# Kernel tuning notes

Measured on AMD Instinct MI355X. Metric: run time of the kernel, lower is better.

Reference implementation:

```python
import jax, jax.numpy as jnp
import numpy as np

B, N, DIM = 4, 4096, 1024
HEADS, DIM_HEAD, BSZ, EPS = 8, 64, 16, 1e-8
INNER = HEADS * DIM_HEAD


def setup_inputs() -> dict:
    key = jax.random.key(0)
    k1, k2, k3 = jax.random.split(key, 3)
    x = jax.random.normal(k1, (B, N, DIM), dtype=jnp.float32)
    # torch nn.Linear weights are [out, in]; scale ~ fan_in^-0.5 for stable exp()
    w_qkv = jax.random.normal(k2, (3 * INNER, DIM), dtype=jnp.float32) * (DIM ** -0.5)
    w_out = jax.random.normal(k3, (DIM, INNER), dtype=jnp.float32) * (INNER ** -0.5)
    b_out = jnp.zeros((DIM,), dtype=jnp.float32)
    return {"x": x, "w_qkv": w_qkv, "w_out": w_out, "b_out": b_out}


def _to_bh(t, b, n):
    # 'b n (h d) -> (b h) n d'
    return t.reshape(b, n, HEADS, DIM_HEAD).transpose(0, 2, 1, 3).reshape(b * HEADS, n, DIM_HEAD)


def _to_blocks(t):
    # 'b (n z) d -> b n z d'
    return t.reshape(t.shape[0], -1, BSZ, DIM_HEAD)


def _calc_Y_and_A(qb, kb, vb):
    S = jnp.einsum('bnid,bnjd->bnij', qb, kb)   # block-local scores
    A = jnp.exp(S)
    y = jnp.einsum('bnij,bnjd->bnid', A, vb)
    return y.reshape(y.shape[0], -1, DIM_HEAD), A.sum(-1).reshape(A.shape[0], -1)


def _hattention(x, w_qkv, w_out, b_out):
    b, n, _ = x.shape
    qkv = x @ w_qkv.T
    q, k, v = jnp.split(qkv, 3, axis=-1)
    q, k, v = (_to_bh(t, b, n) for t in (q, k, v))
    q = q * (DIM_HEAD ** -0.5)

    num_levels = int(np.log2(n // BSZ)) - 1
    qkvs = [(q, k, v)]
    for _ in range(num_levels):
        q = q.reshape(q.shape[0], -1, 2, DIM_HEAD).mean(axis=2)
        k = k.reshape(k.shape[0], -1, 2, DIM_HEAD).mean(axis=2)
        v = v.reshape(v.shape[0], -1, 2, DIM_HEAD).sum(axis=2)
        qkvs.append((q, k, v))
    top_level = qkvs[0]
    coarse_levels = qkvs[1:][::-1]  # coarsest first

    Ys = []
    for (ql, kl, vl) in coarse_levels:
        qb, kb, vb = map(_to_blocks, (ql, kl, vl))
        bh, nb = kb.shape[0], kb.shape[1]
        # flip sibling key blocks: 'b (n r) z d' with r=2 reversed
        kb = kb.reshape(bh, nb // 2, 2, BSZ, DIM_HEAD)[:, :, ::-1].reshape(bh, nb, BSZ, DIM_HEAD)
        Ys.append(_calc_Y_and_A(qb, kb, vb))
    Ys.append(_calc_Y_and_A(*map(_to_blocks, top_level)))

    Y, A = Ys[0]
    for y_l, a_l in Ys[1:]:
        Y = jnp.repeat(Y, 2, axis=1) + y_l
        A = jnp.repeat(A, 2, axis=1) + a_l

    out = Y / (A + EPS)[..., None]
    # '(b h) n d -> b n (h d)'
    out = out.reshape(b, HEADS, n, DIM_HEAD).transpose(0, 2, 1, 3).reshape(b, n, INNER)
    return out @ w_out.T + b_out


def reference(x, w_qkv, w_out, b_out):
    return _hattention(x, w_qkv, w_out, b_out)
```

## Files before the change

### kernel.cpp

```cpp
#include <hip/hip_runtime.h>
#include <hip/hip_bf16.h>


typedef __bf16 bf16x8 __attribute__((ext_vector_type(8)));
typedef float floatx4 __attribute__((ext_vector_type(4)));
typedef unsigned short ushortx8 __attribute__((ext_vector_type(8)));
typedef unsigned int uintx4 __attribute__((ext_vector_type(4)));

#define ROWS_PER_BH 8160

__device__ __forceinline__ void g2lds16(const void* g, void* l) {
  __builtin_amdgcn_global_load_lds(
      (const __attribute__((address_space(1))) void*)g,
      (__attribute__((address_space(3))) void*)l, 16, 0, 0);
}

__device__ __forceinline__ unsigned short f2bu(float x) {
  __hip_bfloat16 h = __float2bfloat16(x);
  return *(unsigned short*)&h;
}
__device__ __forceinline__ float bu2f(unsigned short u) {
  __hip_bfloat16 h = *(__hip_bfloat16*)&u;
  return __bfloat162float(h);
}

__global__ __launch_bounds__(256) void f2b3_kernel(const float* __restrict__ x,
                                                   const float* __restrict__ wq,
                                                   const float* __restrict__ wo,
                                                   __hip_bfloat16* __restrict__ xb,
                                                   __hip_bfloat16* __restrict__ wqb,
                                                   __hip_bfloat16* __restrict__ wob) {
  int i0 = (blockIdx.x * 256 + threadIdx.x) * 8;
  const float* s;
  __hip_bfloat16* d;
  if (i0 < 16777216) {
    s = x + i0; d = xb + i0;
  } else if (i0 < 16777216 + 1572864) {
    s = wq + (i0 - 16777216); d = wqb + (i0 - 16777216);
  } else {
    s = wo + (i0 - 16777216 - 1572864); d = wob + (i0 - 16777216 - 1572864);
  }
  float4 v0 = *(const float4*)s;
  float4 v1 = *(const float4*)(s + 4);
  ushortx8 o;
  o[0] = f2bu(v0.x); o[1] = f2bu(v0.y); o[2] = f2bu(v0.z); o[3] = f2bu(v0.w);
  o[4] = f2bu(v1.x); o[5] = f2bu(v1.y); o[6] = f2bu(v1.z); o[7] = f2bu(v1.w);
  *(ushortx8*)d = o;
}

template <int K>
__device__ __forceinline__ void gemm_core(const unsigned short* __restrict__ A,
                                          const unsigned short* __restrict__ B,
                                          unsigned short* ldsA, unsigned short* ldsB,
                                          int tM, int tN, floatx4 acc[4][4]) {
  const int tid = threadIdx.x;
  const int lane = tid & 63, w = tid >> 6;
  const int wm = w >> 1, wn = w & 1;
  const int lr = lane >> 3;
  const int gch = (lane & 7) ^ lr;
  const unsigned short* Ag = A + (size_t)(tM + w * 32 + lr) * K + gch * 8;
  const unsigned short* Bg = B + (size_t)(tN + w * 32 + lr) * K + gch * 8;
  unsigned short* lA = &ldsA[w * 2048 + lane * 8];
  unsigned short* lB = &ldsB[w * 2048 + lane * 8];

  const int rA = wm * 64 + (lane & 15);
  const int rB = wn * 64 + (lane & 15);
  const int quad = lane >> 4;
  const int sw = lane & 7;

  for (int kt = 0; kt < K; kt += 64) {
    __syncthreads();
#pragma unroll
    for (int c = 0; c < 4; c++) {
      g2lds16(Ag + (size_t)(c * 8) * K + kt, lA + c * 512);
      g2lds16(Bg + (size_t)(c * 8) * K + kt, lB + c * 512);
    }
    __syncthreads();
#pragma unroll
    for (int kk = 0; kk < 2; kk++) {
      bf16x8 af[4], bv[4];
#pragma unroll
      for (int i = 0; i < 4; i++)
        af[i] = *(const bf16x8*)&ldsA[(rA + i * 16) * 64 + (((kk * 4 + quad) ^ sw) * 8)];
#pragma unroll
      for (int j = 0; j < 4; j++)
        bv[j] = *(const bf16x8*)&ldsB[(rB + j * 16) * 64 + (((kk * 4 + quad) ^ sw) * 8)];
#pragma unroll
      for (int i = 0; i < 4; i++)
#pragma unroll
        for (int j = 0; j < 4; j++)
          acc[i][j] = __builtin_amdgcn_mfma_f32_16x16x32_bf16(af[i], bv[j], acc[i][j], 0, 0, 0);
    }
  }
}

__global__ __launch_bounds__(256) void gemm_qkv_kernel(
    const unsigned short* __restrict__ A,
    const unsigned short* __restrict__ B,
    __hip_bfloat16* __restrict__ qp, __hip_bfloat16* __restrict__ kp,
    __hip_bfloat16* __restrict__ vp, int tMoff) {
  __shared__ unsigned short ldsA[128 * 64];
  __shared__ unsigned short ldsB[128 * 64];
  const int lane = threadIdx.x & 63, w = threadIdx.x >> 6;
  const int wm = w >> 1, wn = w & 1;
  const int tM = tMoff + blockIdx.x * 128, tN = blockIdx.y * 128;

  floatx4 acc[4][4];
#pragma unroll
  for (int i = 0; i < 4; i++)
#pragma unroll
    for (int j = 0; j < 4; j++) acc[i][j] = (floatx4){0.f, 0.f, 0.f, 0.f};

  gemm_core<1024>(A, B, ldsA, ldsB, tM, tN, acc);

  const int quad = lane >> 4, m15 = lane & 15;
#pragma unroll
  for (int i = 0; i < 4; i++) {
#pragma unroll
    for (int j = 0; j < 4; j++) {
      const int c = tN + wn * 64 + j * 16 + m15;
      const int tensor = c >> 9;
      const int rem = c & 511;
      const int h = rem >> 6, d = rem & 63;
      __hip_bfloat16* dstbuf = (tensor == 0) ? qp : ((tensor == 1) ? kp : vp);
      const float scale = (tensor == 0) ? 0.125f : 1.0f;
#pragma unroll
      for (int r = 0; r < 4; r++) {
        const int m = tM + wm * 64 + i * 16 + quad * 4 + r;
        const int b = m >> 12, n = m & 4095;
        size_t dst = ((size_t)(b * 8 + h) * ROWS_PER_BH + n) * 64 + d;
        dstbuf[dst] = __float2bfloat16(acc[i][j][r] * scale);
      }
      float s4 = acc[i][j][0] + acc[i][j][1] + acc[i][j][2] + acc[i][j][3];
      s4 += __shfl_xor(s4, 16, 64);
      s4 += __shfl_xor(s4, 32, 64);
      if (quad == 0) {
        const int mrow = tM + wm * 64 + i * 16;
        const int b = mrow >> 12, n4 = (mrow & 4095) >> 4;
        const float val = (tensor == 0) ? s4 * (0.125f / 16.f)
                         : ((tensor == 1) ? s4 * (1.f / 16.f) : s4);
        dstbuf[((size_t)(b * 8 + h) * ROWS_PER_BH + 7680 + n4) * 64 + d] =
            __float2bfloat16(val);
      }
    }
  }
}

__global__ __launch_bounds__(256) void gemm_out_kernel(
    const unsigned short* __restrict__ A,
    const unsigned short* __restrict__ B,
    const float* __restrict__ bias, float* __restrict__ out) {
  __shared__ unsigned short ldsA[128 * 64];
  __shared__ unsigned short ldsB[128 * 64];
  const int lane = threadIdx.x & 63, w = threadIdx.x >> 6;
  const int wm = w >> 1, wn = w & 1;
  const int tM = blockIdx.x * 128, tN = blockIdx.y * 128;

  floatx4 acc[4][4];
#pragma unroll
  for (int i = 0; i < 4; i++)
#pragma unroll
    for (int j = 0; j < 4; j++) acc[i][j] = (floatx4){0.f, 0.f, 0.f, 0.f};

  gemm_core<512>(A, B, ldsA, ldsB, tM, tN, acc);

  const int quad = lane >> 4;
#pragma unroll
  for (int i = 0; i < 4; i++) {
#pragma unroll
    for (int j = 0; j < 4; j++) {
      const int c = tN + wn * 64 + j * 16 + (lane & 15);
      const float bb = bias[c];
#pragma unroll
      for (int r = 0; r < 4; r++) {
        const int m = tM + wm * 64 + i * 16 + quad * 4 + r;
        out[(size_t)m * 1024 + c] = acc[i][j][r] + bb;
      }
    }
  }
}

__device__ __forceinline__ int swzf(int r) { return (r ^ (r >> 3)) & 7; }
__device__ __forceinline__ int sidx(int r, int d) {
  return r * 64 + (((d >> 3) ^ swzf(r)) << 3) + (d & 7);
}
#define VT_SZ 1600

__global__ __launch_bounds__(512, 1) void coarse47_kernel(
    const unsigned short* __restrict__ qp, const unsigned short* __restrict__ kp,
    const unsigned short* __restrict__ vp, __hip_bfloat16* __restrict__ yall,
    float* __restrict__ aall) {
  __shared__ __align__(16) unsigned short qs[256 * 64];
  __shared__ __align__(16) unsigned short ks[256 * 64];
  __shared__ __align__(16) unsigned short vs[256 * 64];
  __shared__ __align__(16) unsigned short vT[8][VT_SZ];

  const int tid = threadIdx.x;
  const int w = tid >> 6, lane = tid & 63;
  const int m = lane & 15, q = lane >> 4;
  const int bh = blockIdx.x;
  const size_t base = (size_t)bh * ROWS_PER_BH;
  const size_t g0 = (base + 7680) * 64;

  unsigned short* vtw = vT[w];

  {
    const int srow = tid >> 3;
    const int sch = (tid & 7) ^ swzf(srow);
    const size_t gofs = (size_t)srow * 64 + sch * 8;
#pragma unroll
    for (int it = 0; it < 4; it++) {
      const size_t gi = g0 + (size_t)it * 4096 + gofs;
      g2lds16(qp + gi, &qs[it * 4096 + tid * 8]);
      g2lds16(kp + gi, &ks[it * 4096 + tid * 8]);
      g2lds16(vp + gi, &vs[it * 4096 + tid * 8]);
    }
  }
  __syncthreads();

  auto attn_block = [&](int level, int blk, bool flip, floatx4 yout[4]) -> float {
    const int kb = flip ? (blk ^ 1) : blk;
    const int Rq = (blk * 16 + m) << level;
    const int Rk = (kb * 16 + m) << level;
    const bf16x8 ka0 = *(const bf16x8*)&ks[sidx(Rk, q * 8)];
    const bf16x8 ka1 = *(const bf16x8*)&ks[sidx(Rk, 32 + q * 8)];
    const bf16x8 qb0 = *(const bf16x8*)&qs[sidx(Rq, q * 8)];
    const bf16x8 qb1 = *(const bf16x8*)&qs[sidx(Rq, 32 + q * 8)];
    const ushortx8 v0 = *(const ushortx8*)&vs[sidx(Rq, q * 16)];
    const ushortx8 v1 = *(const ushortx8*)&vs[sidx(Rq, q * 16 + 8)];
#pragma unroll
    for (int j = 0; j < 8; j++) vtw[q * 16 + (q * 16 + j) * 24 + m] = v0[j];
#pragma unroll
    for (int j = 0; j < 8; j++) vtw[q * 16 + (q * 16 + 8 + j) * 24 + m] = v1[j];

    floatx4 s = (floatx4){0.f, 0.f, 0.f, 0.f};
    s = __builtin_amdgcn_mfma_f32_16x16x32_bf16(ka0, qb0, s, 0, 0, 0);
    s = __builtin_amdgcn_mfma_f32_16x16x32_bf16(ka1, qb1, s, 0, 0, 0);

    unsigned short pb0 = f2bu(__expf(s[0])), pb1 = f2bu(__expf(s[1]));
    unsigned short pb2 = f2bu(__expf(s[2])), pb3 = f2bu(__expf(s[3]));
    float asum = bu2f(pb0) + bu2f(pb1) + bu2f(pb2) + bu2f(pb3);
    asum += __shfl_xor(asum, 16, 64);
    asum += __shfl_xor(asum, 32, 64);

    unsigned int d0 = (unsigned int)pb0 | ((unsigned int)pb1 << 16);
    unsigned int d1 = (unsigned int)pb2 | ((unsigned int)pb3 << 16);
    const int s0l = m + 32 * (q & 1);
    unsigned int u0 = __shfl(d0, s0l, 64);
    unsigned int u1 = __shfl(d1, s0l, 64);
    unsigned int u2 = __shfl(d0, s0l + 16, 64);
    unsigned int u3 = __shfl(d1, s0l + 16, 64);
    union { uintx4 i; bf16x8 b; } pau;
    pau.i = (q < 2) ? (uintx4){u0, u1, u2, u3} : (uintx4){0u, 0u, 0u, 0u};
    const bf16x8 pa = pau.b;

#pragma unroll
    for (int cc = 0; cc < 4; cc++) {
      union { uintx4 i; bf16x8 b; } bvu;
      bvu.i = (uintx4){0u, 0u, 0u, 0u};
      if (q < 2) bvu.b = *(const bf16x8*)&vtw[cc * 16 + (cc * 16 + m) * 24 + q * 8];
      floatx4 y = (floatx4){0.f, 0.f, 0.f, 0.f};
      y = __builtin_amdgcn_mfma_f32_16x16x32_bf16(pa, bvu.b, y, 0, 0, 0);
      yout[cc] = y;
    }
    return asum;
  };

  auto pyr = [&](int l) {
    const int nOut = 256 >> l;
    for (int e = tid; e < nOut * 32; e += 512) {
      const int i = e >> 5, dp = (e & 31) * 2;
      const int ra = i << l, rb = ra + (1 << (l - 1));
      const int ia = sidx(ra, dp), ib = sidx(rb, dp);
      unsigned short q0 = f2bu(0.5f * (bu2f(qs[ia]) + bu2f(qs[ib])));
      unsigned short q1 = f2bu(0.5f * (bu2f(qs[ia + 1]) + bu2f(qs[ib + 1])));
      unsigned short k0 = f2bu(0.5f * (bu2f(ks[ia]) + bu2f(ks[ib])));
      unsigned short k1 = f2bu(0.5f * (bu2f(ks[ia + 1]) + bu2f(ks[ib + 1])));
      unsigned short v0 = f2bu(bu2f(vs[ia]) + bu2f(vs[ib]));
      unsigned short v1 = f2bu(bu2f(vs[ia + 1]) + bu2f(vs[ib + 1]));
      qs[ia] = q0; qs[ia + 1] = q1;
      ks[ia] = k0; ks[ia + 1] = k1;
      vs[ia] = v0; vs[ia + 1] = v1;
    }
  };

  auto emit = [&](int ro, int blk, const floatx4 yt[4], float a) {
    const size_t arow = base + ro + blk * 16;
    if (q == 0) aall[arow + m] = a;
#pragma unroll
    for (int cc = 0; cc < 4; cc++)
#pragma unroll
      for (int r = 0; r < 4; r++)
        yall[(arow + q * 4 + r) * 64 + cc * 16 + m] = __float2bfloat16(yt[cc][r]);
  };

  {
    floatx4 yt[4];
#pragma unroll
    for (int t = 0; t < 2; t++) {
      const int blk = w + t * 8;
      float a = attn_block(0, blk, true, yt);
      emit(7680, blk, yt, a);
    }
  }
  __syncthreads();
  pyr(1);
  __syncthreads();
  {
    floatx4 yt[4];
    float a = attn_block(1, w, true, yt);
    emit(7936, w, yt, a);
  }
  __syncthreads();
  pyr(2);
  __syncthreads();
  if (w < 4) {
    floatx4 yt[4];
    float a = attn_block(2, w, true, yt);
    emit(8064, w, yt, a);
  }
  __syncthreads();
  pyr(3);
  __syncthreads();
  if (w < 2) {
    floatx4 yt[4];
    float a = attn_block(3, w, true, yt);
    emit(8128, w, yt, a);
  }
}

__global__ __launch_bounds__(512, 1) void fused03_kernel(
    const unsigned short* __restrict__ qp, const unsigned short* __restrict__ kp,
    const unsigned short* __restrict__ vp, const unsigned short* __restrict__ yall,
    const float* __restrict__ aall, __hip_bfloat16* __restrict__ Ub) {
  __shared__ __align__(16) unsigned short qs[256 * 64];
  __shared__ __align__(16) unsigned short ks[256 * 64];
  __shared__ __align__(16) unsigned short vs[256 * 64];
  __shared__ unsigned short ylds[224 * 72];
  __shared__ float alds[480];
  __shared__ __align__(16) unsigned short vT[8][VT_SZ];

  const int tid = threadIdx.x;
  const int w = tid >> 6, lane = tid & 63;
  const int m = lane & 15, q = lane >> 4;
  const int c = blockIdx.x, bh = blockIdx.y;
  const size_t base = (size_t)bh * ROWS_PER_BH;
  const size_t g0 = (base + c * 256) * 64;

  unsigned short* vtw = vT[w];

  {
    const int srow = tid >> 3;
    const int sch = (tid & 7) ^ swzf(srow);
    const size_t gofs = (size_t)srow * 64 + sch * 8;
#pragma unroll
    for (int it = 0; it < 4; it++) {
      const size_t gi = g0 + (size_t)it * 4096 + gofs;
      g2lds16(qp + gi, &qs[it * 4096 + tid * 8]);
      g2lds16(kp + gi, &ks[it * 4096 + tid * 8]);
      g2lds16(vp + gi, &vs[it * 4096 + tid * 8]);
    }
  }
  __syncthreads();

  auto attn_block = [&](int level, int blk, bool flip, floatx4 yout[4]) -> float {
    const int kb = flip ? (blk ^ 1) : blk;
    const int Rq = (blk * 16 + m) << level;
    const int Rk = (kb * 16 + m) << level;
    const bf16x8 ka0 = *(const bf16x8*)&ks[sidx(Rk, q * 8)];
    const bf16x8 ka1 = *(const bf16x8*)&ks[sidx(Rk, 32 + q * 8)];
    const bf16x8 qb0 = *(const bf16x8*)&qs[sidx(Rq, q * 8)];
    const bf16x8 qb1 = *(const bf16x8*)&qs[sidx(Rq, 32 + q * 8)];
    const ushortx8 v0 = *(const ushortx8*)&vs[sidx(Rq, q * 16)];
    const ushortx8 v1 = *(const ushortx8*)&vs[sidx(Rq, q * 16 + 8)];
#pragma unroll
    for (int j = 0; j < 8; j++) vtw[q * 16 + (q * 16 + j) * 24 + m] = v0[j];
#pragma unroll
    for (int j = 0; j < 8; j++) vtw[q * 16 + (q * 16 + 8 + j) * 24 + m] = v1[j];

    floatx4 s = (floatx4){0.f, 0.f, 0.f, 0.f};
    s = __builtin_amdgcn_mfma_f32_16x16x32_bf16(ka0, qb0, s, 0, 0, 0);
    s = __builtin_amdgcn_mfma_f32_16x16x32_bf16(ka1, qb1, s, 0, 0, 0);

    unsigned short pb0 = f2bu(__expf(s[0])), pb1 = f2bu(__expf(s[1]));
    unsigned short pb2 = f2bu(__expf(s[2])), pb3 = f2bu(__expf(s[3]));
    float asum = bu2f(pb0) + bu2f(pb1) + bu2f(pb2) + bu2f(pb3);
    asum += __shfl_xor(asum, 16, 64);
    asum += __shfl_xor(asum, 32, 64);

    unsigned int d0 = (unsigned int)pb0 | ((unsigned int)pb1 << 16);
    unsigned int d1 = (unsigned int)pb2 | ((unsigned int)pb3 << 16);
    const int s0l = m + 32 * (q & 1);
    unsigned int u0 = __shfl(d0, s0l, 64);
    unsigned int u1 = __shfl(d1, s0l, 64);
    unsigned int u2 = __shfl(d0, s0l + 16, 64);
    unsigned int u3 = __shfl(d1, s0l + 16, 64);
    union { uintx4 i; bf16x8 b; } pau;
    pau.i = (q < 2) ? (uintx4){u0, u1, u2, u3} : (uintx4){0u, 0u, 0u, 0u};
    const bf16x8 pa = pau.b;

#pragma unroll
    for (int cc = 0; cc < 4; cc++) {
      union { uintx4 i; bf16x8 b; } bvu;
      bvu.i = (uintx4){0u, 0u, 0u, 0u};
      if (q < 2) bvu.b = *(const bf16x8*)&vtw[cc * 16 + (cc * 16 + m) * 24 + q * 8];
      floatx4 y = (floatx4){0.f, 0.f, 0.f, 0.f};
      y = __builtin_amdgcn_mfma_f32_16x16x32_bf16(pa, bvu.b, y, 0, 0, 0);
      yout[cc] = y;
    }
    return asum;
  };

  auto pyr = [&](int l) {
    const int nOut = 256 >> l;
    for (int e = tid; e < nOut * 32; e += 512) {
      const int i = e >> 5, dp = (e & 31) * 2;
      const int ra = i << l, rb = ra + (1 << (l - 1));
      const int ia = sidx(ra, dp), ib = sidx(rb, dp);
      unsigned short q0 = f2bu(0.5f * (bu2f(qs[ia]) + bu2f(qs[ib])));
      unsigned short q1 = f2bu(0.5f * (bu2f(qs[ia + 1]) + bu2f(qs[ib + 1])));
      unsigned short k0 = f2bu(0.5f * (bu2f(ks[ia]) + bu2f(ks[ib])));
      unsigned short k1 = f2bu(0.5f * (bu2f(ks[ia + 1]) + bu2f(ks[ib + 1])));
      unsigned short v0 = f2bu(bu2f(vs[ia]) + bu2f(vs[ib]));
      unsigned short v1 = f2bu(bu2f(vs[ia + 1]) + bu2f(vs[ib + 1]));
      qs[ia] = q0; qs[ia + 1] = q1;
      ks[ia] = k0; ks[ia + 1] = k1;
      vs[ia] = v0; vs[ia + 1] = v1;
    }
  };

  floatx4 y0reg[2][4];
#pragma unroll
  for (int t = 0; t < 2; t++) {
    const int blk = w + t * 8;
    float a0 = attn_block(0, blk, false, y0reg[t]);
    if (q == 0) alds[224 + blk * 16 + m] = a0;
  }
  __syncthreads();

  pyr(1);
  __syncthreads();
  {
    floatx4 yt[4];
    const int blk = w;
    float a = attn_block(1, blk, true, yt);
    if (q == 0) alds[blk * 16 + m] = a;
#pragma unroll
    for (int cc = 0; cc < 4; cc++)
#pragma unroll
      for (int r = 0; r < 4; r++)
        ylds[(blk * 16 + q * 4 + r) * 72 + cc * 16 + m] = f2bu(yt[cc][r]);
  }
  __syncthreads();
  pyr(2);
  __syncthreads();
  if (w < 4) {
    floatx4 yt[4];
    const int blk = w;
    float a = attn_block(2, blk, true, yt);
    if (q == 0) alds[128 + blk * 16 + m] = a;
#pragma unroll
    for (int cc = 0; cc < 4; cc++)
#pragma unroll
      for (int r = 0; r < 4; r++)
        ylds[(128 + blk * 16 + q * 4 + r) * 72 + cc * 16 + m] = f2bu(yt[cc][r]);
  }
  __syncthreads();
  pyr(3);
  __syncthreads();
  if (w < 2) {
    floatx4 yt[4];
    const int blk = w;
    float a = attn_block(3, blk, true, yt);
    if (q == 0) alds[192 + blk * 16 + m] = a;
#pragma unroll
    for (int cc = 0; cc < 4; cc++)
#pragma unroll
      for (int r = 0; r < 4; r++)
        ylds[(192 + blk * 16 + q * 4 + r) * 72 + cc * 16 + m] = f2bu(yt[cc][r]);
  }
  __syncthreads();

  const int bO = bh >> 3, hO = bh & 7;
#pragma unroll
  for (int t = 0; t < 2; t++) {
    const int blk = w + t * 8;
    const int i4 = c * 16 + blk;
    const size_t r4 = base + 7680 + i4;
    const size_t r5 = base + 7936 + (i4 >> 1);
    const size_t r6 = base + 8064 + (i4 >> 2);
    const size_t r7 = base + 8128 + (i4 >> 3);
    const float acoarse = aall[r4] + aall[r5] + aall[r6] + aall[r7];

    float inv[4];
#pragma unroll
    for (int r = 0; r < 4; r++) {
      const int row = blk * 16 + q * 4 + r;
      const float atot = alds[224 + row] + alds[row >> 1] +
                         alds[128 + (row >> 2)] + alds[192 + (row >> 3)] +
                         acoarse + 1e-8f;
      inv[r] = 1.0f / atot;
    }

#pragma unroll
    for (int cc = 0; cc < 4; cc++) {
      const int col = cc * 16 + m;
      const float yc = bu2f(yall[r4 * 64 + col]) + bu2f(yall[r5 * 64 + col]) +
                       bu2f(yall[r6 * 64 + col]) + bu2f(yall[r7 * 64 + col]);
#pragma unroll
      for (int r = 0; r < 4; r++) {
        const int row = blk * 16 + q * 4 + r;
        const float num = y0reg[t][cc][r] + bu2f(ylds[(row >> 1) * 72 + col]) +
                          bu2f(ylds[(128 + (row >> 2)) * 72 + col]) +
                          bu2f(ylds[(192 + (row >> 3)) * 72 + col]) + yc;
        Ub[((size_t)bO * 4096 + c * 256 + row) * 512 + hO * 64 + col] =
            __float2bfloat16(num * inv[r]);
      }
    }
  }
}

extern "C" void kernel_launch(void* const* d_in, const int* in_sizes, int n_in,
                              void* d_out, int out_size, void* d_ws, size_t ws_size,
                              hipStream_t stream) {
  const float* x     = (const float*)d_in[0];
  const float* w_qkv = (const float*)d_in[1];
  const float* w_out = (const float*)d_in[2];
  const float* b_out = (const float*)d_in[3];
  float* out = (float*)d_out;

  char* ws = (char*)d_ws;
  __hip_bfloat16* xb    = (__hip_bfloat16*)(ws + 0);
  __hip_bfloat16* wqkvb = (__hip_bfloat16*)(ws + 33554432);
  __hip_bfloat16* wob   = (__hip_bfloat16*)(ws + 36700160);
  __hip_bfloat16* qp    = (__hip_bfloat16*)(ws + 37748736);
  __hip_bfloat16* kp    = (__hip_bfloat16*)(ws + 71172096);
  __hip_bfloat16* vp    = (__hip_bfloat16*)(ws + 104595456);
  __hip_bfloat16* yall  = (__hip_bfloat16*)(ws + 138018816);
  float* aall           = (float*)(ws + 171442176);
  __hip_bfloat16* Ub    = (__hip_bfloat16*)(ws + 172486656);

  f2b3_kernel<<<9216, 256, 0, stream>>>(x, w_qkv, w_out, xb, wqkvb, wob);

  gemm_qkv_kernel<<<dim3(64, 12), 256, 0, stream>>>(
      (const unsigned short*)xb, (const unsigned short*)wqkvb, qp, kp, vp, 0);
  gemm_qkv_kernel<<<dim3(64, 12), 256, 0, stream>>>(
      (const unsigned short*)xb, (const unsigned short*)wqkvb, qp, kp, vp, 8192);

  coarse47_kernel<<<32, 512, 0, stream>>>(
      (const unsigned short*)qp, (const unsigned short*)kp,
      (const unsigned short*)vp, yall, aall);

  fused03_kernel<<<dim3(16, 32), 512, 0, stream>>>(
      (const unsigned short*)qp, (const unsigned short*)kp,
      (const unsigned short*)vp, (const unsigned short*)yall, aall, Ub);

  gemm_out_kernel<<<dim3(128, 8), 256, 0, stream>>>(
      (const unsigned short*)Ub, (const unsigned short*)wob, b_out, out);
}
```

Baseline: 271.1 us.

## Compute pyramid levels 1-3 in QKV GEMM epilogue and read them from global

The QKV GEMM epilogue now writes pooled q/k/v for levels 1, 2 and 3 (pairs, quads, octets) as well as level 4, using partial sums of the accumulator fragments. The fused03 kernel therefore drops its LDS staging of 256 rows and the in-LDS pyramid reductions with their barriers, and loads each level's blocks straight from global memory. This frees most of its shared memory, so launch bounds allow 4 blocks per CU, and levels 2 and 3 now run concurrently on different waves. The two QKV GEMM launches are merged into one. In exchange the GEMM epilogue issues more scattered bf16 stores, and the pooled values are formed from fp32 accumulators rather than from bf16-rounded rows.

```diff
diff --git a/kernel.cpp b/kernel.cpp
--- a/kernel.cpp
+++ b/kernel.cpp
@@ -94,16 +94,18 @@
   }
 }
 
+__constant__ int LVLOFF[8] = {0, 4096, 6144, 7168, 7680, 7936, 8064, 8128};
+
 __global__ __launch_bounds__(256) void gemm_qkv_kernel(
     const unsigned short* __restrict__ A,
     const unsigned short* __restrict__ B,
     __hip_bfloat16* __restrict__ qp, __hip_bfloat16* __restrict__ kp,
-    __hip_bfloat16* __restrict__ vp, int tMoff) {
+    __hip_bfloat16* __restrict__ vp) {
   __shared__ unsigned short ldsA[128 * 64];
   __shared__ unsigned short ldsB[128 * 64];
   const int lane = threadIdx.x & 63, w = threadIdx.x >> 6;
   const int wm = w >> 1, wn = w & 1;
-  const int tM = tMoff + blockIdx.x * 128, tN = blockIdx.y * 128;
+  const int tM = blockIdx.x * 128, tN = blockIdx.y * 128;
 
   floatx4 acc[4][4];
 #pragma unroll
@@ -131,16 +133,35 @@
         size_t dst = ((size_t)(b * 8 + h) * ROWS_PER_BH + n) * 64 + d;
         dstbuf[dst] = __float2bfloat16(acc[i][j][r] * scale);
       }
-      float s4 = acc[i][j][0] + acc[i][j][1] + acc[i][j][2] + acc[i][j][3];
-      s4 += __shfl_xor(s4, 16, 64);
-      s4 += __shfl_xor(s4, 32, 64);
+      const float s2a = acc[i][j][0] + acc[i][j][1];
+      const float s2b = acc[i][j][2] + acc[i][j][3];
+      const float s4v = s2a + s2b;
+      const float s8v = s4v + __shfl_xor(s4v, 16, 64);
+      const float s16v = s8v + __shfl_xor(s8v, 32, 64);
+      const int mg = tM + wm * 64 + i * 16;
+      const int b = mg >> 12, nb = mg & 4095;
+      const size_t rb = (size_t)(b * 8 + h) * ROWS_PER_BH;
+      const bool isv = (tensor == 2);
+      {
+        const float dv = isv ? 1.f : 0.5f;
+        const int n1 = (nb >> 1) + quad * 2;
+        dstbuf[(rb + 4096 + n1) * 64 + d] = __float2bfloat16(s2a * dv * scale);
+        dstbuf[(rb + 4096 + n1 + 1) * 64 + d] = __float2bfloat16(s2b * dv * scale);
+      }
+      {
+        const float dv = isv ? 1.f : 0.25f;
+        dstbuf[(rb + 6144 + (nb >> 2) + quad) * 64 + d] =
+            __float2bfloat16(s4v * dv * scale);
+      }
+      if ((quad & 1) == 0) {
+        const float dv = isv ? 1.f : 0.125f;
+        dstbuf[(rb + 7168 + (nb >> 3) + (quad >> 1)) * 64 + d] =
+            __float2bfloat16(s8v * dv * scale);
+      }
       if (quad == 0) {
-        const int mrow = tM + wm * 64 + i * 16;
-        const int b = mrow >> 12, n4 = (mrow & 4095) >> 4;
-        const float val = (tensor == 0) ? s4 * (0.125f / 16.f)
-                         : ((tensor == 1) ? s4 * (1.f / 16.f) : s4);
-        dstbuf[((size_t)(b * 8 + h) * ROWS_PER_BH + 7680 + n4) * 64 + d] =
-            __float2bfloat16(val);
+        const float dv = isv ? 1.f : 0.0625f;
+        dstbuf[(rb + 7680 + (nb >> 4)) * 64 + d] =
+            __float2bfloat16(s16v * dv * scale);
       }
     }
   }
@@ -218,8 +239,8 @@
   }
   __syncthreads();
 
-  auto attn_block = [&](int level, int blk, bool flip, floatx4 yout[4]) -> float {
-    const int kb = flip ? (blk ^ 1) : blk;
+  auto attn_block = [&](int level, int blk, floatx4 yout[4]) -> float {
+    const int kb = blk ^ 1;
     const int Rq = (blk * 16 + m) << level;
     const int Rk = (kb * 16 + m) << level;
     const bf16x8 ka0 = *(const bf16x8*)&ks[sidx(Rk, q * 8)];
@@ -270,8 +291,8 @@
     const int nOut = 256 >> l;
     for (int e = tid; e < nOut * 32; e += 512) {
       const int i = e >> 5, dp = (e & 31) * 2;
-      const int ra = i << l, rb = ra + (1 << (l - 1));
-      const int ia = sidx(ra, dp), ib = sidx(rb, dp);
+      const int ra = i << l, rb2 = ra + (1 << (l - 1));
+      const int ia = sidx(ra, dp), ib = sidx(rb2, dp);
       unsigned short q0 = f2bu(0.5f * (bu2f(qs[ia]) + bu2f(qs[ib])));
       unsigned short q1 = f2bu(0.5f * (bu2f(qs[ia + 1]) + bu2f(qs[ib + 1])));
       unsigned short k0 = f2bu(0.5f * (bu2f(ks[ia]) + bu2f(ks[ib])));
@@ -299,7 +320,7 @@
 #pragma unroll
     for (int t = 0; t < 2; t++) {
       const int blk = w + t * 8;
-      float a = attn_block(0, blk, true, yt);
+      float a = attn_block(0, blk, yt);
       emit(7680, blk, yt, a);
     }
   }
@@ -308,7 +329,7 @@
   __syncthreads();
   {
     floatx4 yt[4];
-    float a = attn_block(1, w, true, yt);
+    float a = attn_block(1, w, yt);
     emit(7936, w, yt, a);
   }
   __syncthreads();
@@ -316,7 +337,7 @@
   __syncthreads();
   if (w < 4) {
     floatx4 yt[4];
-    float a = attn_block(2, w, true, yt);
+    float a = attn_block(2, w, yt);
     emit(8064, w, yt, a);
   }
   __syncthreads();
@@ -324,18 +345,15 @@
   __syncthreads();
   if (w < 2) {
     floatx4 yt[4];
-    float a = attn_block(3, w, true, yt);
+    float a = attn_block(3, w, yt);
     emit(8128, w, yt, a);
   }
 }
 
-__global__ __launch_bounds__(512, 1) void fused03_kernel(
+__global__ __launch_bounds__(512, 4) void fused03_kernel(
     const unsigned short* __restrict__ qp, const unsigned short* __restrict__ kp,
     const unsigned short* __restrict__ vp, const unsigned short* __restrict__ yall,
     const float* __restrict__ aall, __hip_bfloat16* __restrict__ Ub) {
-  __shared__ __align__(16) unsigned short qs[256 * 64];
-  __shared__ __align__(16) unsigned short ks[256 * 64];
-  __shared__ __align__(16) unsigned short vs[256 * 64];
   __shared__ unsigned short ylds[224 * 72];
   __shared__ float alds[480];
   __shared__ __align__(16) unsigned short vT[8][VT_SZ];
@@ -345,42 +363,24 @@
   const int m = lane & 15, q = lane >> 4;
   const int c = blockIdx.x, bh = blockIdx.y;
   const size_t base = (size_t)bh * ROWS_PER_BH;
-  const size_t g0 = (base + c * 256) * 64;
 
   unsigned short* vtw = vT[w];
 
-  {
-    const int srow = tid >> 3;
-    const int sch = (tid & 7) ^ swzf(srow);
-    const size_t gofs = (size_t)srow * 64 + sch * 8;
-#pragma unroll
-    for (int it = 0; it < 4; it++) {
-      const size_t gi = g0 + (size_t)it * 4096 + gofs;
-      g2lds16(qp + gi, &qs[it * 4096 + tid * 8]);
-      g2lds16(kp + gi, &ks[it * 4096 + tid * 8]);
-      g2lds16(vp + gi, &vs[it * 4096 + tid * 8]);
-    }
-  }
-  __syncthreads();
-
-  auto attn_block = [&](int level, int blk, bool flip, floatx4 yout[4]) -> float {
-    const int kb = flip ? (blk ^ 1) : blk;
-    const int Rq = (blk * 16 + m) << level;
-    const int Rk = (kb * 16 + m) << level;
-    const bf16x8 ka0 = *(const bf16x8*)&ks[sidx(Rk, q * 8)];
-    const bf16x8 ka1 = *(const bf16x8*)&ks[sidx(Rk, 32 + q * 8)];
-    const bf16x8 qb0 = *(const bf16x8*)&qs[sidx(Rq, q * 8)];
-    const bf16x8 qb1 = *(const bf16x8*)&qs[sidx(Rq, 32 + q * 8)];
-    const ushortx8 v0 = *(const ushortx8*)&vs[sidx(Rq, q * 16)];
-    const ushortx8 v1 = *(const ushortx8*)&vs[sidx(Rq, q * 16 + 8)];
+  auto attn_g = [&](size_t qb, size_t kb, floatx4 yout[4]) -> float {
+    const bf16x8 ka0 = *(const bf16x8*)(kp + kb + m * 64 + q * 8);
+    const bf16x8 ka1 = *(const bf16x8*)(kp + kb + m * 64 + 32 + q * 8);
+    const bf16x8 qv0 = *(const bf16x8*)(qp + qb + m * 64 + q * 8);
+    const bf16x8 qv1 = *(const bf16x8*)(qp + qb + m * 64 + 32 + q * 8);
+    const ushortx8 v0 = *(const ushortx8*)(vp + qb + m * 64 + q * 16);
+    const ushortx8 v1 = *(const ushortx8*)(vp + qb + m * 64 + q * 16 + 8);
 #pragma unroll
     for (int j = 0; j < 8; j++) vtw[q * 16 + (q * 16 + j) * 24 + m] = v0[j];
 #pragma unroll
     for (int j = 0; j < 8; j++) vtw[q * 16 + (q * 16 + 8 + j) * 24 + m] = v1[j];
 
     floatx4 s = (floatx4){0.f, 0.f, 0.f, 0.f};
-    s = __builtin_amdgcn_mfma_f32_16x16x32_bf16(ka0, qb0, s, 0, 0, 0);
-    s = __builtin_amdgcn_mfma_f32_16x16x32_bf16(ka1, qb1, s, 0, 0, 0);
+    s = __builtin_amdgcn_mfma_f32_16x16x32_bf16(ka0, qv0, s, 0, 0, 0);
+    s = __builtin_amdgcn_mfma_f32_16x16x32_bf16(ka1, qv1, s, 0, 0, 0);
 
     unsigned short pb0 = f2bu(__expf(s[0])), pb1 = f2bu(__expf(s[1]));
     unsigned short pb2 = f2bu(__expf(s[2])), pb3 = f2bu(__expf(s[3]));
@@ -411,67 +411,41 @@
     return asum;
   };
 
-  auto pyr = [&](int l) {
-    const int nOut = 256 >> l;
-    for (int e = tid; e < nOut * 32; e += 512) {
-      const int i = e >> 5, dp = (e & 31) * 2;
-      const int ra = i << l, rb = ra + (1 << (l - 1));
-      const int ia = sidx(ra, dp), ib = sidx(rb, dp);
-      unsigned short q0 = f2bu(0.5f * (bu2f(qs[ia]) + bu2f(qs[ib])));
-      unsigned short q1 = f2bu(0.5f * (bu2f(qs[ia + 1]) + bu2f(qs[ib + 1])));
-      unsigned short k0 = f2bu(0.5f * (bu2f(ks[ia]) + bu2f(ks[ib])));
-      unsigned short k1 = f2bu(0.5f * (bu2f(ks[ia + 1]) + bu2f(ks[ib + 1])));
-      unsigned short v0 = f2bu(bu2f(vs[ia]) + bu2f(vs[ib]));
-      unsigned short v1 = f2bu(bu2f(vs[ia + 1]) + bu2f(vs[ib + 1]));
-      qs[ia] = q0; qs[ia + 1] = q1;
-      ks[ia] = k0; ks[ia + 1] = k1;
-      vs[ia] = v0; vs[ia + 1] = v1;
-    }
+  auto lvbase = [&](int l, int blk) -> size_t {
+    return (base + LVLOFF[l] + c * (256 >> l) + blk * 16) * 64;
   };
 
   floatx4 y0reg[2][4];
 #pragma unroll
   for (int t = 0; t < 2; t++) {
     const int blk = w + t * 8;
-    float a0 = attn_block(0, blk, false, y0reg[t]);
+    const size_t qb = lvbase(0, blk);
+    float a0 = attn_g(qb, qb, y0reg[t]);
     if (q == 0) alds[224 + blk * 16 + m] = a0;
   }
-  __syncthreads();
-
-  pyr(1);
-  __syncthreads();
   {
     floatx4 yt[4];
-    const int blk = w;
-    float a = attn_block(1, blk, true, yt);
-    if (q == 0) alds[blk * 16 + m] = a;
+    float a = attn_g(lvbase(1, w), lvbase(1, w ^ 1), yt);
+    if (q == 0) alds[w * 16 + m] = a;
 #pragma unroll
     for (int cc = 0; cc < 4; cc++)
 #pragma unroll
       for (int r = 0; r < 4; r++)
-        ylds[(blk * 16 + q * 4 + r) * 72 + cc * 16 + m] = f2bu(yt[cc][r]);
-  }
-  __syncthreads();
-  pyr(2);
-  __syncthreads();
+        ylds[(w * 16 + q * 4 + r) * 72 + cc * 16 + m] = f2bu(yt[cc][r]);
+  }
   if (w < 4) {
     floatx4 yt[4];
-    const int blk = w;
-    float a = attn_block(2, blk, true, yt);
-    if (q == 0) alds[128 + blk * 16 + m] = a;
+    float a = attn_g(lvbase(2, w), lvbase(2, w ^ 1), yt);
+    if (q == 0) alds[128 + w * 16 + m] = a;
 #pragma unroll
     for (int cc = 0; cc < 4; cc++)
 #pragma unroll
       for (int r = 0; r < 4; r++)
-        ylds[(128 + blk * 16 + q * 4 + r) * 72 + cc * 16 + m] = f2bu(yt[cc][r]);
-  }
-  __syncthreads();
-  pyr(3);
-  __syncthreads();
-  if (w < 2) {
-    floatx4 yt[4];
-    const int blk = w;
-    float a = attn_block(3, blk, true, yt);
+        ylds[(128 + w * 16 + q * 4 + r) * 72 + cc * 16 + m] = f2bu(yt[cc][r]);
+  } else if (w < 6) {
+    floatx4 yt[4];
+    const int blk = w - 4;
+    float a = attn_g(lvbase(3, blk), lvbase(3, blk ^ 1), yt);
     if (q == 0) alds[192 + blk * 16 + m] = a;
 #pragma unroll
     for (int cc = 0; cc < 4; cc++)
@@ -542,10 +516,8 @@
 
   f2b3_kernel<<<9216, 256, 0, stream>>>(x, w_qkv, w_out, xb, wqkvb, wob);
 
-  gemm_qkv_kernel<<<dim3(64, 12), 256, 0, stream>>>(
-      (const unsigned short*)xb, (const unsigned short*)wqkvb, qp, kp, vp, 0);
-  gemm_qkv_kernel<<<dim3(64, 12), 256, 0, stream>>>(
-      (const unsigned short*)xb, (const unsigned short*)wqkvb, qp, kp, vp, 8192);
+  gemm_qkv_kernel<<<dim3(128, 12), 256, 0, stream>>>(
+      (const unsigned short*)xb, (const unsigned short*)wqkvb, qp, kp, vp);
 
   coarse47_kernel<<<32, 512, 0, stream>>>(
       (const unsigned short*)qp, (const unsigned short*)kp,
```

New measurement: 256.5 us. 5.4% less time.
